# Performance work log

Measured on AMD Instinct MI355X. Metric: run time of the kernel, lower is better.

The kernel has to match this reference:

```python
import jax, jax.numpy as jnp
import numpy as np

B, C, K, F = 16, 64, 128, 6
HORIZON_S = 3.0  # conflict_horizon_s default
EPS = 1e-06


def setup_inputs() -> dict:
    rng = np.random.default_rng(0)
    # base adjacency: sparse random directed graph, zero diagonal
    A = (rng.random((B, K, K)) < 0.05).astype(np.float32)
    A[:, np.arange(K), np.arange(K)] = 0.0
    # candidates: exactly one unordered-pair edit (state in {0:none,1:i->j,2:j->i})
    cand = np.repeat(A[:, None], C, axis=1).copy()
    i = rng.integers(0, K - 1, (B, C))
    j = i + 1 + (rng.integers(0, K - 1, (B, C)) % (K - 1 - i))
    state = rng.integers(0, 3, (B, C))
    bidx = np.arange(B)[:, None] * np.ones((1, C), dtype=np.int64)
    cidx = np.ones((B, 1), dtype=np.int64) * np.arange(C)[None, :]
    cand[bidx, cidx, i, j] = (state == 1).astype(np.float32)
    cand[bidx, cidx, j, i] = (state == 2).astype(np.float32)
    cand[:, 0] = A  # candidate 0 is NOOP (keep A_t)
    # agent features: (x, y, yaw, vx, vy, pad)
    feat = rng.normal(size=(B, K, F)).astype(np.float32)
    feat[..., 0:2] *= 20.0  # spread positions over ~40m
    mask = (rng.random((B, K)) > 0.1).astype(np.float32)
    return {
        "A_t": jnp.asarray(A),
        "candidate_A": jnp.asarray(cand),
        "agent_feat": jnp.asarray(feat),
        "agent_mask": jnp.asarray(mask),
    }


def _edit_tokens(A_t, candidate_A):
    # vectorized version of EBSTM.extract_edit_tokens
    Bn, Cn, Kn, _ = candidate_A.shape
    base = A_t > 0.5                      # [B,K,K]
    cb = candidate_A > 0.5                # [B,C,K,K]
    diff = cb != base[:, None]            # [B,C,K,K]
    upper = jnp.triu(jnp.ones((Kn, Kn), dtype=bool), k=1)
    pairdiff = (diff | jnp.swapaxes(diff, -1, -2)) & upper
    flat = pairdiff.reshape(Bn, Cn, Kn * Kn)
    changed = flat.any(-1)                # [B,C]
    idx = jnp.argmax(flat, axis=-1)       # first changed pair in row-major (i,j) order
    i = idx // Kn
    j = idx % Kn
    barange = jnp.arange(Bn)[:, None]
    carange = jnp.arange(Cn)[None, :]
    b_ij = base[barange, i, j]
    b_ji = base[barange, j, i]
    c_ij = cb[barange, carange, i, j]
    c_ji = cb[barange, carange, j, i]
    prev = jnp.where(b_ij & ~b_ji, 1, jnp.where(b_ji & ~b_ij, 2, 0))
    nxt = jnp.where(c_ij & ~c_ji, 1, jnp.where(c_ji & ~c_ij, 2, 0))
    tokens = jnp.stack([i, j, prev, nxt], axis=-1).astype(jnp.int32)
    return tokens * changed[..., None].astype(jnp.int32)


def _relation_state3(cb):
    # cb: bool [B,C,K,K]
    at = jnp.swapaxes(cb, -1, -2)
    return ((cb & ~at).astype(jnp.int32) * 1
            + (~cb & at).astype(jnp.int32) * 2
            + (cb & at).astype(jnp.int32) * 3)


def _batched_acyclic(cb, agent_mask):
    # vectorized Kahn zero-indegree peel, matching EBSTM._is_acyclic semantics:
    #  - indegree counts edges from ALL sources (valid or not)
    #  - only valid nodes are ever removed
    #  - special case: <=1 valid node is acyclic
    Bn, Cn, Kn, _ = cb.shape
    valid = (agent_mask > 0.5)[:, None, :]           # [B,1,K]
    Ai = cb.astype(jnp.int32)                        # [B,C,K,K]
    indeg = Ai.sum(axis=-2) * valid.astype(jnp.int32)  # [B,C,K]
    removed = jnp.zeros((Bn, Cn, Kn), dtype=bool)

    def body(t, carry):
        indeg, removed = carry
        rem = valid & (~removed) & (indeg == 0)
        dec = jnp.einsum('bci,bcij->bcj', rem.astype(jnp.int32), Ai)
        return indeg - dec, removed | rem

    indeg, removed = jax.lax.fori_loop(0, Kn, body, (indeg, removed))
    vcount = valid.astype(jnp.int32).sum(-1)          # [B,1]
    return (removed.astype(jnp.int32).sum(-1) == vcount) | (vcount <= 1)


def _pair_dists(agent_feat):
    pos = agent_feat[..., 0:2]
    vel = agent_feat[..., 3:5]
    # _pair_distance: d[b,i,j] = |pos_i - pos_j|
    d = jnp.linalg.norm(pos[:, :, None] - pos[:, None, :], axis=-1)
    # _pair_closest_approach_distance: r[b,i,j] = pos_j - pos_i
    r = pos[:, None, :] - pos[:, :, None]
    v = vel[:, None, :] - vel[:, :, None]
    vv = (v * v).sum(-1)
    rv = (r * v).sum(-1)
    t_star = jnp.clip(-rv / (vv + EPS), 0.0, HORIZON_S)
    dmin = jnp.linalg.norm(r + v * t_star[..., None], axis=-1)
    eye = jnp.eye(dmin.shape[-1], dtype=bool)[None]
    dmin = jnp.where(eye, jnp.inf, dmin)
    return jnp.stack([d, dmin], axis=0)  # [2,B,K,K]


def reference(A_t, candidate_A, agent_feat, agent_mask):
    cb = candidate_A > 0.5
    tokens = _edit_tokens(A_t, candidate_A)          # [B,C,4] int32
    rel = _relation_state3(cb)                       # [B,C,K,K] int32
    acyclic = _batched_acyclic(cb, agent_mask)       # [B,C] bool
    dists = _pair_dists(agent_feat)                  # [2,B,K,K] float32
    return tokens, rel, acyclic, dists
```

## Files before the change

### kernel.cpp

```cpp
#include <hip/hip_runtime.h>
#include <cstdint>
#include <math.h>

#define KN 128
#define BATCH 16
#define CAND 64

typedef float vfloat4 __attribute__((ext_vector_type(4)));

static constexpr size_t TOK_OFF = 0;
static constexpr size_t REL_OFF = (size_t)BATCH * CAND * 4;
static constexpr size_t ACY_OFF = REL_OFF + (size_t)BATCH * CAND * KN * KN;
static constexpr size_t DST_OFF = ACY_OFF + (size_t)BATCH * CAND;

#define DIAG_BIG 1.0e30f

__global__ __launch_bounds__(256) void fused_kernel(const float* __restrict__ A_t,
                                                    const float* __restrict__ cand,
                                                    const float* __restrict__ feat,
                                                    const float* __restrict__ mask,
                                                    float* __restrict__ out) {
    __shared__ uint32_t adj[KN][5];
    __shared__ uint32_t baseB[KN][4];
    __shared__ int      indeg[KN];
    __shared__ uint32_t validW[4];
    __shared__ uint32_t remW[4];
    __shared__ uint32_t removedW[4];
    __shared__ int      minIdx;

    const int t    = threadIdx.x;
    const int lane = t & 63;
    const int wave = t >> 6;
    const int bc   = blockIdx.x;
    const int b    = bc >> 6;

    const float* cptr = cand + (size_t)bc * (KN * KN);
    const float* aptr = A_t + (size_t)b * (KN * KN);

    if (t == 0) minIdx = 0x7fffffff;
    if (t < 4)  removedW[t] = 0;

    if (wave < 2) {
        float mv = mask[b * KN + wave * 64 + lane];
        unsigned long long m = __ballot(mv > 0.5f);
        if (lane == 0) {
            validW[wave * 2]     = (uint32_t)m;
            validW[wave * 2 + 1] = (uint32_t)(m >> 32);
        }
    }

    for (int m = 0; m < 16; ++m) {
        int rowPair = m * 4 + wave;
        int r   = rowPair * 2 + (lane >> 5);
        int sub = lane & 31;
        const float4 v = ((const float4*)(aptr + (size_t)r * KN))[sub];
        uint32_t nib = (v.x > 0.5f ? 1u : 0u) | (v.y > 0.5f ? 2u : 0u) |
                       (v.z > 0.5f ? 4u : 0u) | (v.w > 0.5f ? 8u : 0u);
        uint32_t word = nib << (4 * (sub & 7));
        word |= __shfl_xor(word, 1);
        word |= __shfl_xor(word, 2);
        word |= __shfl_xor(word, 4);
        if ((lane & 7) == 0) baseB[r][sub >> 3] = word;
    }

    for (int m = 0; m < 16; ++m) {
        int rowPair = m * 4 + wave;
        int r   = rowPair * 2 + (lane >> 5);
        int sub = lane & 31;
        vfloat4 v = __builtin_nontemporal_load(((const vfloat4*)(cptr + (size_t)r * KN)) + sub);
        uint32_t nib = (v.x > 0.5f ? 1u : 0u) | (v.y > 0.5f ? 2u : 0u) |
                       (v.z > 0.5f ? 4u : 0u) | (v.w > 0.5f ? 8u : 0u);
        uint32_t word = nib << (4 * (sub & 7));
        word |= __shfl_xor(word, 1);
        word |= __shfl_xor(word, 2);
        word |= __shfl_xor(word, 4);
        if ((lane & 7) == 0) adj[r][sub >> 3] = word;
    }

    {
        int bi = 2 * bc + (t >> 7);
        int b2 = bi >> 7, i = bi & 127, j = t & 127;
        const float* fi = feat + (size_t)bi * 6;
        const float* fj = feat + (size_t)(b2 * KN + j) * 6;
        float pix = fi[0], piy = fi[1], vix = fi[3], viy = fi[4];
        float pjx = fj[0], pjy = fj[1], vjx = fj[3], vjy = fj[4];
        float dx = pix - pjx, dy = piy - pjy;
        float d = sqrtf(dx * dx + dy * dy);
        float rx = pjx - pix, ry = pjy - piy;
        float vx = vjx - vix, vy = vjy - viy;
        float vv = vx * vx + vy * vy;
        float rv = rx * vx + ry * vy;
        float ts = fminf(fmaxf(-rv / (vv + 1e-6f), 0.0f), 3.0f);
        float mx = rx + vx * ts, my = ry + vy * ts;
        float dmin = (i == j) ? DIAG_BIG : sqrtf(mx * mx + my * my);
        float* o = out + DST_OFF;
        __builtin_nontemporal_store(d,    o + (size_t)(b2 * KN + i) * KN + j);
        __builtin_nontemporal_store(dmin, o + (size_t)((BATCH + b2) * KN + i) * KN + j);
    }
    __syncthreads();

    {
        float* relp = out + REL_OFF + (size_t)bc * (KN * KN);
        for (int m = 0; m < 16; ++m) {
            int q  = t + 256 * m;
            int i  = q >> 5;
            int j0 = (q & 31) * 4;
            uint32_t wij = adj[i][j0 >> 5];
            int sh = j0 & 31;
            uint32_t iw = i >> 5, ib = i & 31;
            uint32_t t0 = (adj[j0 + 0][iw] >> ib) & 1u;
            uint32_t t1 = (adj[j0 + 1][iw] >> ib) & 1u;
            uint32_t t2 = (adj[j0 + 2][iw] >> ib) & 1u;
            uint32_t t3 = (adj[j0 + 3][iw] >> ib) & 1u;
            vfloat4 o;
            o.x = (float)(((wij >> (sh + 0)) & 1u) + 2u * t0);
            o.y = (float)(((wij >> (sh + 1)) & 1u) + 2u * t1);
            o.z = (float)(((wij >> (sh + 2)) & 1u) + 2u * t2);
            o.w = (float)(((wij >> (sh + 3)) & 1u) + 2u * t3);
            __builtin_nontemporal_store(o, ((vfloat4*)relp) + q);
        }
    }

    for (int idx = t; idx < 512; idx += 256) {
        int i = idx >> 2, k = idx & 3;
        uint32_t diff = adj[i][k] ^ baseB[i][k];
        if (diff) {
            int base = k * 32;
            uint32_t up, low;
            if (i < base)            { up = diff; low = 0u; }
            else if (i >= base + 31) { up = 0u; low = (i > base + 31) ? diff : (diff & 0x7fffffffu); }
            else {
                int s = i - base;
                up  = diff & (0xffffffffu << (s + 1));
                low = diff & ((1u << s) - 1u);
            }
            int c1 = 0x7fffffff, c2 = 0x7fffffff;
            if (up)  c1 = (i << 7) | (base + __builtin_ctz(up));
            if (low) { int cc = base + __builtin_ctz(low); c2 = (cc << 7) | i; }
            int cm = min(c1, c2);
            if (cm != 0x7fffffff) atomicMin(&minIdx, cm);
        }
    }

    if (t < KN) {
        uint32_t jw = t >> 5, jb = t & 31;
        int s = 0;
        for (int i = 0; i < KN; ++i) s += (adj[i][jw] >> jb) & 1u;
        bool valid = (validW[jw] >> jb) & 1u;
        indeg[t] = valid ? s : 0;
    }
    __syncthreads();

    if (t == 0) {
        float* tok = out + TOK_OFF + (size_t)bc * 4;
        int mi = minIdx;
        if (mi != 0x7fffffff) {
            int i = mi >> 7, j = mi & 127;
            uint32_t b_ij = (baseB[i][j >> 5] >> (j & 31)) & 1u;
            uint32_t b_ji = (baseB[j][i >> 5] >> (i & 31)) & 1u;
            uint32_t c_ij = (adj[i][j >> 5] >> (j & 31)) & 1u;
            uint32_t c_ji = (adj[j][i >> 5] >> (i & 31)) & 1u;
            int prev = (b_ij && !b_ji) ? 1 : ((b_ji && !b_ij) ? 2 : 0);
            int nxt  = (c_ij && !c_ji) ? 1 : ((c_ji && !c_ij) ? 2 : 0);
            tok[0] = (float)i; tok[1] = (float)j; tok[2] = (float)prev; tok[3] = (float)nxt;
        } else {
            tok[0] = 0.f; tok[1] = 0.f; tok[2] = 0.f; tok[3] = 0.f;
        }
    }

    for (int it = 0; it < KN; ++it) {
        bool rem = false;
        if (t < KN) {
            uint32_t jw = t >> 5, jb = t & 31;
            bool valid   = (validW[jw] >> jb) & 1u;
            bool removed = (removedW[jw] >> jb) & 1u;
            rem = valid && !removed && (indeg[t] == 0);
        }
        unsigned long long m = __ballot(rem);
        if (wave < 2 && lane == 0) {
            remW[wave * 2]     = (uint32_t)m;
            remW[wave * 2 + 1] = (uint32_t)(m >> 32);
        }
        __syncthreads();
        uint32_t r0 = remW[0], r1 = remW[1], r2 = remW[2], r3 = remW[3];
        if ((r0 | r1 | r2 | r3) == 0u) break;
        if (t < 4) removedW[t] |= remW[t];
        if (t < KN) {
            uint32_t jw = t >> 5, jb = t & 31;
            int dec = 0;
            uint32_t rw[4] = {r0, r1, r2, r3};
            for (int w = 0; w < 4; ++w) {
                uint32_t mm = rw[w];
                while (mm) {
                    int i = w * 32 + __builtin_ctz(mm);
                    mm &= mm - 1;
                    dec += (adj[i][jw] >> jb) & 1u;
                }
            }
            indeg[t] -= dec;
        }
        __syncthreads();
    }
    __syncthreads();

    if (t == 0) {
        int rc = __popc(removedW[0]) + __popc(removedW[1]) + __popc(removedW[2]) + __popc(removedW[3]);
        int vc = __popc(validW[0]) + __popc(validW[1]) + __popc(validW[2]) + __popc(validW[3]);
        out[ACY_OFF + bc] = ((rc == vc) || (vc <= 1)) ? 1.0f : 0.0f;
    }
}

extern "C" void kernel_launch(void* const* d_in, const int* in_sizes, int n_in,
                              void* d_out, int out_size, void* d_ws, size_t ws_size,
                              hipStream_t stream) {
    const float* A_t  = (const float*)d_in[0];
    const float* cand = (const float*)d_in[1];
    const float* feat = (const float*)d_in[2];
    const float* mask = (const float*)d_in[3];
    float* out = (float*)d_out;

    fused_kernel<<<BATCH * CAND, 256, 0, stream>>>(A_t, cand, feat, mask, out);
}
```

Baseline: 137.7 us.

## Transpose adjacency in LDS, split indegree count, defer relation stores

Adds a word-transposed copy of the candidate adjacency bitmask so each relation-state output reads its four transpose words with one vector LDS load instead of four scattered ones. The indegree column count is split across all 256 threads in two halves rather than 128 threads serially scanning 128 rows. The relation-state store loop moves after the token write, just before the topological-sort loop, and one extra barrier is added. The candidate load also switches from a nontemporal load to a normal cached load. The goal is less LDS bank conflict and serial work on the pre-sort path, at the cost of extra shared memory and an added synchronisation.

After: 137.1 us. Within noise of the previous version (-0.4%).

```diff
diff --git a/kernel.cpp b/kernel.cpp
--- a/kernel.cpp
+++ b/kernel.cpp
@@ -21,7 +21,9 @@
                                                     const float* __restrict__ mask,
                                                     float* __restrict__ out) {
     __shared__ uint32_t adj[KN][5];
+    __shared__ uint32_t adjW[4][KN];
     __shared__ uint32_t baseB[KN][4];
+    __shared__ int      indegP[2][KN];
     __shared__ int      indeg[KN];
     __shared__ uint32_t validW[4];
     __shared__ uint32_t remW[4];
@@ -67,7 +69,7 @@
         int rowPair = m * 4 + wave;
         int r   = rowPair * 2 + (lane >> 5);
         int sub = lane & 31;
-        vfloat4 v = __builtin_nontemporal_load(((const vfloat4*)(cptr + (size_t)r * KN)) + sub);
+        const float4 v = ((const float4*)(cptr + (size_t)r * KN))[sub];
         uint32_t nib = (v.x > 0.5f ? 1u : 0u) | (v.y > 0.5f ? 2u : 0u) |
                        (v.z > 0.5f ? 4u : 0u) | (v.w > 0.5f ? 8u : 0u);
         uint32_t word = nib << (4 * (sub & 7));
@@ -99,26 +101,18 @@
     }
     __syncthreads();
 
+    for (int w = t; w < 512; w += 256) {
+        int iw = w >> 7, j = w & 127;
+        adjW[iw][j] = adj[j][iw];
+    }
+
     {
-        float* relp = out + REL_OFF + (size_t)bc * (KN * KN);
-        for (int m = 0; m < 16; ++m) {
-            int q  = t + 256 * m;
-            int i  = q >> 5;
-            int j0 = (q & 31) * 4;
-            uint32_t wij = adj[i][j0 >> 5];
-            int sh = j0 & 31;
-            uint32_t iw = i >> 5, ib = i & 31;
-            uint32_t t0 = (adj[j0 + 0][iw] >> ib) & 1u;
-            uint32_t t1 = (adj[j0 + 1][iw] >> ib) & 1u;
-            uint32_t t2 = (adj[j0 + 2][iw] >> ib) & 1u;
-            uint32_t t3 = (adj[j0 + 3][iw] >> ib) & 1u;
-            vfloat4 o;
-            o.x = (float)(((wij >> (sh + 0)) & 1u) + 2u * t0);
-            o.y = (float)(((wij >> (sh + 1)) & 1u) + 2u * t1);
-            o.z = (float)(((wij >> (sh + 2)) & 1u) + 2u * t2);
-            o.w = (float)(((wij >> (sh + 3)) & 1u) + 2u * t3);
-            __builtin_nontemporal_store(o, ((vfloat4*)relp) + q);
-        }
+        int j = t & 127, half = t >> 7;
+        uint32_t jw = j >> 5, jb = j & 31;
+        int s = 0;
+        int i0 = half * 64;
+        for (int i = i0; i < i0 + 64; ++i) s += (adj[i][jw] >> jb) & 1u;
+        indegP[half][j] = s;
     }
 
     for (int idx = t; idx < 512; idx += 256) {
@@ -141,15 +135,13 @@
             if (cm != 0x7fffffff) atomicMin(&minIdx, cm);
         }
     }
+    __syncthreads();
 
     if (t < KN) {
         uint32_t jw = t >> 5, jb = t & 31;
-        int s = 0;
-        for (int i = 0; i < KN; ++i) s += (adj[i][jw] >> jb) & 1u;
         bool valid = (validW[jw] >> jb) & 1u;
-        indeg[t] = valid ? s : 0;
-    }
-    __syncthreads();
+        indeg[t] = valid ? (indegP[0][t] + indegP[1][t]) : 0;
+    }
 
     if (t == 0) {
         float* tok = out + TOK_OFF + (size_t)bc * 4;
@@ -167,6 +159,26 @@
             tok[0] = 0.f; tok[1] = 0.f; tok[2] = 0.f; tok[3] = 0.f;
         }
     }
+
+    {
+        float* relp = out + REL_OFF + (size_t)bc * (KN * KN);
+        for (int m = 0; m < 16; ++m) {
+            int q  = t + 256 * m;
+            int i  = q >> 5;
+            int j0 = (q & 31) * 4;
+            uint32_t wij = adj[i][j0 >> 5];
+            int sh = j0 & 31;
+            uint32_t iw = i >> 5, ib = i & 31;
+            const uint4 wt = *(const uint4*)&adjW[iw][j0];
+            vfloat4 o;
+            o.x = (float)(((wij >> (sh + 0)) & 1u) + 2u * ((wt.x >> ib) & 1u));
+            o.y = (float)(((wij >> (sh + 1)) & 1u) + 2u * ((wt.y >> ib) & 1u));
+            o.z = (float)(((wij >> (sh + 2)) & 1u) + 2u * ((wt.z >> ib) & 1u));
+            o.w = (float)(((wij >> (sh + 3)) & 1u) + 2u * ((wt.w >> ib) & 1u));
+            __builtin_nontemporal_store(o, ((vfloat4*)relp) + q);
+        }
+    }
+    __syncthreads();
 
     for (int it = 0; it < KN; ++it) {
         bool rem = false;
```
